# Kernel optimization log

Hardware: AMD Instinct MI355X
Metric: run time of the kernel (lower is better)

Reference implementation:

```python
import jax, jax.numpy as jnp
import numpy as np
from jax import lax

B, T, SDIM, ADIM, HDIM, NH, NBLK, MAXT = 4, 512, 64, 32, 512, 8, 6, 4096
DFF = 4 * HDIM
S = 3 * T  # (num_state_tokens + 1) * context_len
DH = HDIM // NH


def _layernorm(x, g, b, eps=1e-5):
    m = jnp.mean(x, axis=-1, keepdims=True)
    v = jnp.mean((x - m) ** 2, axis=-1, keepdims=True)
    return (x - m) * lax.rsqrt(v + eps) * g + b


def setup_inputs() -> dict:
    key = jax.random.key(0)
    ks = iter(jax.random.split(key, 40))

    def nrm(shape, scale=0.02):
        return jax.random.normal(next(ks), shape, jnp.float32) * scale

    inp = {
        "timesteps": jax.random.randint(next(ks), (B, T), 0, MAXT),
        "state_0": jax.random.normal(next(ks), (B, T, SDIM), jnp.float32),
        "state_1": jax.random.normal(next(ks), (B, T, SDIM), jnp.float32),
        "actions": jax.random.normal(next(ks), (B, T, ADIM), jnp.float32),
        # embeddings / input projections
        "time_emb": nrm((MAXT, HDIM)),
        "Ws": nrm((SDIM, HDIM)), "bs": jnp.zeros((HDIM,), jnp.float32),
        "Wa": nrm((ADIM, HDIM)), "ba": jnp.zeros((HDIM,), jnp.float32),
        # stacked per-block transformer params (leading axis = n_blocks)
        "Wq": nrm((NBLK, HDIM, HDIM)), "bq": jnp.zeros((NBLK, HDIM), jnp.float32),
        "Wk": nrm((NBLK, HDIM, HDIM)), "bk": jnp.zeros((NBLK, HDIM), jnp.float32),
        "Wv": nrm((NBLK, HDIM, HDIM)), "bv": jnp.zeros((NBLK, HDIM), jnp.float32),
        "Wo": nrm((NBLK, HDIM, HDIM)), "bo": jnp.zeros((NBLK, HDIM), jnp.float32),
        "W1": nrm((NBLK, HDIM, DFF)), "b1": jnp.zeros((NBLK, DFF), jnp.float32),
        "W2": nrm((NBLK, DFF, HDIM)), "b2": jnp.zeros((NBLK, HDIM), jnp.float32),
        "ln1_g": jnp.ones((NBLK, HDIM), jnp.float32), "ln1_b": jnp.zeros((NBLK, HDIM), jnp.float32),
        "ln2_g": jnp.ones((NBLK, HDIM), jnp.float32), "ln2_b": jnp.zeros((NBLK, HDIM), jnp.float32),
        # embed layernorm + action head
        "eln_g": jnp.ones((HDIM,), jnp.float32), "eln_b": jnp.zeros((HDIM,), jnp.float32),
        "Wp": nrm((HDIM, ADIM)), "bp": jnp.zeros((ADIM,), jnp.float32),
    }
    return inp


def reference(timesteps, state_0, state_1, actions, time_emb, Ws, bs, Wa, ba,
              Wq, bq, Wk, bk, Wv, bv, Wo, bo, W1, b1, W2, b2,
              ln1_g, ln1_b, ln2_g, ln2_b, eln_g, eln_b, Wp, bp):
    te = time_emb[timesteps]                       # (B, T, H)
    s0 = state_0 @ Ws + bs + te                    # shared state embedding
    s1 = state_1 @ Ws + bs + te
    ae = actions @ Wa + ba + te
    # interleave: (B, T, 3, H) -> (B, 3T, H), token order [s0, s1, a] per timestep
    h = jnp.stack([s0, s1, ae], axis=2).reshape(B, S, HDIM)
    h = _layernorm(h, eln_g, eln_b)

    causal = jnp.tril(jnp.ones((S, S), dtype=bool))
    scale = 1.0 / float(DH) ** 0.5

    def block(x, p):
        wq, bq_, wk, bk_, wv, bv_, wo, bo_, w1, b1_, w2, b2_, g1, be1, g2, be2 = p
        q = (x @ wq + bq_).reshape(B, S, NH, DH)
        k = (x @ wk + bk_).reshape(B, S, NH, DH)
        v = (x @ wv + bv_).reshape(B, S, NH, DH)
        scores = jnp.einsum('bihd,bjhd->bhij', q, k) * scale
        scores = jnp.where(causal, scores, -jnp.inf)
        attn = jax.nn.softmax(scores, axis=-1)
        ctx = jnp.einsum('bhij,bjhd->bihd', attn, v).reshape(B, S, HDIM)
        x = x + (ctx @ wo + bo_)
        x = _layernorm(x, g1, be1)
        mlp = jax.nn.gelu(x @ w1 + b1_, approximate=False) @ w2 + b2_
        x = _layernorm(x + mlp, g2, be2)
        return x, None

    h, _ = lax.scan(block, h,
                    (Wq, bq, Wk, bk, Wv, bv, Wo, bo, W1, b1, W2, b2,
                     ln1_g, ln1_b, ln2_g, ln2_b))

    h = h.reshape(B, T, 3, HDIM)                   # (B, T, num_tokens, H)
    act_in = h[:, :, 1]                            # token index -2 = last state token
    return act_in @ Wp + bp                        # (B, T, act_dim)
```

## Files before the change

### kernel.cpp

```cpp
#include <hip/hip_runtime.h>
#include <hip/hip_bf16.h>
#include <math.h>

#define BB 4
#define TT 512
#define SDIM 64
#define ADIM 32
#define HDIM 512
#define NH 8
#define NBLK 6
#define DFF 2048
#define SS 1536
#define DH 64
#define MS (BB*SS)

typedef __attribute__((ext_vector_type(8))) __bf16 bf16x8;
typedef __attribute__((ext_vector_type(4))) float f32x4;

__device__ __forceinline__ __bf16 f2b(float x) { return (__bf16)x; }

__device__ __forceinline__ void gll16(const void* g, void* l) {
    __builtin_amdgcn_global_load_lds(
        (const __attribute__((address_space(1))) unsigned int*)g,
        (__attribute__((address_space(3))) unsigned int*)l, 16, 0, 0);
}

__global__ __launch_bounds__(512) void embed_ln_kernel(
    const int* __restrict__ timesteps,
    const float* __restrict__ state0, const float* __restrict__ state1,
    const float* __restrict__ actions, const float* __restrict__ time_emb,
    const float* __restrict__ Ws, const float* __restrict__ bs,
    const float* __restrict__ Wa, const float* __restrict__ ba,
    const float* __restrict__ eg, const float* __restrict__ eb,
    __bf16* __restrict__ h_bf)
{
    __shared__ float xs[8][64];
    __shared__ float acc_s[8][512];
    __shared__ int tss[8];
    int c = blockIdx.x, t = blockIdx.y, b = blockIdx.z;
    int i0 = c * 8;
    int tid = threadIdx.x;
    int K = (t == 2) ? ADIM : SDIM;
    int ksh = (t == 2) ? 5 : 6;
    const float* W    = (t == 2) ? Wa : Ws;
    const float* bias = (t == 2) ? ba : bs;
    const float* src  = (t == 0) ? state0  + ((size_t)(b*TT + i0)) * SDIM
                      : (t == 1) ? state1  + ((size_t)(b*TT + i0)) * SDIM
                                 : actions + ((size_t)(b*TT + i0)) * ADIM;

    if (tid < 8) tss[tid] = timesteps[b*TT + i0 + tid];
    for (int idx = tid; idx < 8 * K; idx += 512) {
        int r = idx >> ksh, kk = idx & (K - 1);
        xs[r][kk] = src[r * K + kk];
    }
    __syncthreads();

    float acc[8];
    #pragma unroll
    for (int r = 0; r < 8; ++r)
        acc[r] = bias[tid] + time_emb[(size_t)tss[r] * HDIM + tid];
    for (int kk = 0; kk < K; ++kk) {
        float w = W[(size_t)kk * HDIM + tid];
        #pragma unroll
        for (int r = 0; r < 8; ++r) acc[r] += xs[r][kk] * w;
    }
    #pragma unroll
    for (int r = 0; r < 8; ++r) acc_s[r][tid] = acc[r];
    __syncthreads();

    int w = tid >> 6, lane = tid & 63;
    float4 p0 = *(const float4*)&acc_s[w][lane * 8];
    float4 p1 = *(const float4*)&acc_s[w][lane * 8 + 4];
    float v[8] = {p0.x, p0.y, p0.z, p0.w, p1.x, p1.y, p1.z, p1.w};
    float s = 0.f, sq = 0.f;
    #pragma unroll
    for (int u = 0; u < 8; ++u) { s += v[u]; sq += v[u] * v[u]; }
    #pragma unroll
    for (int off = 1; off < 64; off <<= 1) { s += __shfl_xor(s, off); sq += __shfl_xor(sq, off); }
    float mean = s * (1.f / HDIM);
    float var  = sq * (1.f / HDIM) - mean * mean;
    float inv  = rsqrtf(var + 1e-5f);
    float4 g0 = *(const float4*)(eg + lane * 8), g1 = *(const float4*)(eg + lane * 8 + 4);
    float4 b0 = *(const float4*)(eb + lane * 8), b1 = *(const float4*)(eb + lane * 8 + 4);
    float gg[8] = {g0.x, g0.y, g0.z, g0.w, g1.x, g1.y, g1.z, g1.w};
    float bbv[8] = {b0.x, b0.y, b0.z, b0.w, b1.x, b1.y, b1.z, b1.w};
    __bf16 o8[8];
    #pragma unroll
    for (int u = 0; u < 8; ++u) o8[u] = f2b((v[u] - mean) * inv * gg[u] + bbv[u]);
    int row = b * SS + (i0 + w) * 3 + t;
    *(uint4*)(h_bf + (size_t)row * HDIM + lane * 8) = *(uint4*)o8;
}

template<bool TWO>
__global__ __launch_bounds__(256) void ln_add_kernel(
    __bf16* __restrict__ h_bf, const __bf16* __restrict__ ya,
    const __bf16* __restrict__ yb,
    const float* __restrict__ g, const float* __restrict__ bvec)
{
    int w = threadIdx.x >> 6, lane = threadIdx.x & 63;
    int row = blockIdx.x * 4 + w;
    size_t base = (size_t)row * HDIM + lane * 8;
    bf16x8 h8 = *(const bf16x8*)(h_bf + base);
    bf16x8 a8 = *(const bf16x8*)(ya + base);
    bf16x8 b8;
    if (TWO) b8 = *(const bf16x8*)(yb + base);
    float v[8], s = 0.f, sq = 0.f;
    #pragma unroll
    for (int u = 0; u < 8; ++u) {
        v[u] = (float)h8[u] + (float)a8[u] + (TWO ? (float)b8[u] : 0.f);
        s += v[u]; sq += v[u] * v[u];
    }
    #pragma unroll
    for (int off = 1; off < 64; off <<= 1) { s += __shfl_xor(s, off); sq += __shfl_xor(sq, off); }
    float mean = s * (1.f / HDIM);
    float var  = sq * (1.f / HDIM) - mean * mean;
    float inv  = rsqrtf(var + 1e-5f);
    float4 g0 = *(const float4*)(g + lane * 8), g1 = *(const float4*)(g + lane * 8 + 4);
    float4 b0 = *(const float4*)(bvec + lane * 8), b1 = *(const float4*)(bvec + lane * 8 + 4);
    float gg[8] = {g0.x, g0.y, g0.z, g0.w, g1.x, g1.y, g1.z, g1.w};
    float bbv[8] = {b0.x, b0.y, b0.z, b0.w, b1.x, b1.y, b1.z, b1.w};
    __bf16 o8[8];
    #pragma unroll
    for (int u = 0; u < 8; ++u) o8[u] = f2b((v[u] - mean) * inv * gg[u] + bbv[u]);
    *(uint4*)(h_bf + base) = *(uint4*)o8;
}

__global__ __launch_bounds__(256) void pack_kernel(
    const float* __restrict__ Wq, const float* __restrict__ Wk,
    const float* __restrict__ Wv, const float* __restrict__ Wo,
    const float* __restrict__ W1, const float* __restrict__ W2,
    const float* __restrict__ bq_, const float* __restrict__ bk_, const float* __restrict__ bv_,
    __bf16* __restrict__ wqkvT, __bf16* __restrict__ woT,
    __bf16* __restrict__ w1T, __bf16* __restrict__ w2T, float* __restrict__ biasq)
{
    int lyr = blockIdx.y;
    const float* wq = Wq + (size_t)lyr * HDIM * HDIM;
    const float* wk = Wk + (size_t)lyr * HDIM * HDIM;
    const float* wv = Wv + (size_t)lyr * HDIM * HDIM;
    const float* wo = Wo + (size_t)lyr * HDIM * HDIM;
    const float* w1 = W1 + (size_t)lyr * HDIM * DFF;
    const float* w2 = W2 + (size_t)lyr * DFF * HDIM;
    const float* bqL = bq_ + (size_t)lyr * HDIM;
    const float* bkL = bk_ + (size_t)lyr * HDIM;
    const float* bvL = bv_ + (size_t)lyr * HDIM;
    wqkvT += (size_t)lyr * 1536 * 512;
    woT   += (size_t)lyr * 512 * 512;
    w1T   += (size_t)lyr * 2048 * 512;
    w2T   += (size_t)lyr * 512 * 2048;
    biasq += (size_t)lyr * 1536;

    int bid = blockIdx.x;
    int tid = threadIdx.x;
    if (bid == 768) {
        for (int i = tid; i < 1536; i += 256)
            biasq[i] = (i < 512) ? bqL[i] : ((i < 1024) ? bkL[i-512] : bvL[i-1024]);
        return;
    }
    __shared__ float Ls[64][65];
    const float* src; __bf16* dst; int K, N, kt, nt;
    if (bid < 192) {
        int sec = bid / 64, t = bid % 64;
        src = (sec == 0) ? wq : (sec == 1) ? wk : wv;
        dst = wqkvT + (size_t)sec * 512 * 512;
        K = 512; N = 512; nt = t >> 3; kt = t & 7;
    } else if (bid < 256) {
        int t = bid - 192; src = wo; dst = woT; K = 512; N = 512; nt = t >> 3; kt = t & 7;
    } else if (bid < 512) {
        int t = bid - 256; src = w1; dst = w1T; K = 512; N = 2048; nt = t >> 3; kt = t & 7;
    } else {
        int t = bid - 512; src = w2; dst = w2T; K = 2048; N = 512; nt = t & 7; kt = t >> 3;
    }
    int k0 = kt * 64, n0 = nt * 64;
    int rr = tid >> 4, cc = (tid & 15) * 4;
    #pragma unroll
    for (int p = 0; p < 4; ++p) {
        float4 v = *(const float4*)(src + (size_t)(k0 + rr + p*16) * N + n0 + cc);
        Ls[rr + p*16][cc] = v.x; Ls[rr + p*16][cc+1] = v.y;
        Ls[rr + p*16][cc+2] = v.z; Ls[rr + p*16][cc+3] = v.w;
    }
    __syncthreads();
    int nn = tid >> 3, kc = (tid & 7) * 8;
    #pragma unroll
    for (int p = 0; p < 2; ++p) {
        __bf16 t8[8];
        #pragma unroll
        for (int t2 = 0; t2 < 8; ++t2) t8[t2] = f2b(Ls[kc + t2][nn + p*32]);
        *(uint4*)(dst + (size_t)(n0 + nn + p*32) * K + k0 + kc) = *(uint4*)t8;
    }
}

template<int MT, bool VTMODE>
__global__ __launch_bounds__(256) void gemm_mfma(
    const __bf16* __restrict__ A, const __bf16* __restrict__ Bt,
    const float* __restrict__ bias, __bf16* __restrict__ C,
    __bf16* __restrict__ VTout,
    int N, int Ksub, int lda, int ldb, int ldc, int gelu, size_t cSplitStride)
{
    constexpr int MI = MT / 32;
    constexpr int SMB = 2*MT*64 + 2*128*64;
    __shared__ __align__(16) char sm[SMB];
    __bf16* As = (__bf16*)sm;
    __bf16* Bs = (__bf16*)(sm + 2*MT*64);
    int tid = threadIdx.x;
    int wave = tid >> 6, lane = tid & 63;
    int l15 = lane & 15, quad = lane >> 4;
    int wy = wave >> 1, wx = wave & 1;
    int m0 = blockIdx.y * MT, n0 = blockIdx.x * 128;
    int zs = blockIdx.z;
    int kbase = zs * Ksub;
    C += (size_t)zs * cSplitStride;

    int srow = lane >> 2;
    int clog = (lane & 3) ^ ((lane >> 3) & 3);
    int pchunk = (quad ^ ((l15 >> 1) & 3)) * 8;

    f32x4 acc[MI][4];
    #pragma unroll
    for (int i = 0; i < MI; ++i)
        #pragma unroll
        for (int j = 0; j < 4; ++j) acc[i][j] = (f32x4){0.f,0.f,0.f,0.f};

    const __bf16* Abase = A  + (size_t)m0 * lda + kbase + clog * 8;
    const __bf16* Bbase = Bt + (size_t)n0 * ldb + kbase + clog * 8;
    int NK = Ksub >> 5;

    #pragma unroll
    for (int q = 0; q < MT/64; ++q) {
        int r0 = (wave * (MT/64) + q) * 16;
        gll16(Abase + (size_t)(r0 + srow) * lda, As + r0*32);
    }
    #pragma unroll
    for (int q = 0; q < 2; ++q) {
        int r0 = (wave * 2 + q) * 16;
        gll16(Bbase + (size_t)(r0 + srow) * ldb, Bs + r0*32);
    }

    for (int kt = 0; kt < NK; ++kt) {
        int buf = kt & 1;
        __syncthreads();
        if (kt + 1 < NK) {
            int k0 = (kt + 1) << 5;
            #pragma unroll
            for (int q = 0; q < MT/64; ++q) {
                int r0 = (wave * (MT/64) + q) * 16;
                gll16(Abase + (size_t)(r0 + srow) * lda + k0, As + ((buf^1)*MT + r0)*32);
            }
            #pragma unroll
            for (int q = 0; q < 2; ++q) {
                int r0 = (wave * 2 + q) * 16;
                gll16(Bbase + (size_t)(r0 + srow) * ldb + k0, Bs + ((buf^1)*128 + r0)*32);
            }
        }
        bf16x8 af[MI], bf[4];
        #pragma unroll
        for (int i = 0; i < MI; ++i)
            af[i] = *(const bf16x8*)&As[(buf*MT + wy*(MT/2) + i*16 + l15)*32 + pchunk];
        #pragma unroll
        for (int j = 0; j < 4; ++j)
            bf[j] = *(const bf16x8*)&Bs[(buf*128 + wx*64 + j*16 + l15)*32 + pchunk];
        #pragma unroll
        for (int i = 0; i < MI; ++i)
            #pragma unroll
            for (int j = 0; j < 4; ++j)
                acc[i][j] = __builtin_amdgcn_mfma_f32_16x16x32_bf16(af[i], bf[j], acc[i][j], 0, 0, 0);
    }

    if (VTMODE && n0 >= 1024) {
        __syncthreads();
        __bf16* T = (__bf16*)sm;
        #pragma unroll
        for (int j = 0; j < 4; ++j) {
            int dl = wx*64 + j*16 + l15;
            float bv = bias[n0 + dl];
            int x31 = dl & 31;
            #pragma unroll
            for (int i = 0; i < MI; ++i) {
                int sc = wy*16 + i*4 + quad;
                int phys = sc ^ x31;
                __bf16 v4[4];
                #pragma unroll
                for (int r = 0; r < 4; ++r) v4[r] = f2b(acc[i][j][r] + bv);
                *(uint2*)(T + dl*128 + phys*4) = *(uint2*)v4;
            }
        }
        __syncthreads();
        int dl = tid >> 1, sh = (tid & 1) * 64;
        int dglob = n0 - 1024 + dl;
        int bb = m0 / SS, srel = m0 - bb*SS;
        __bf16* vb = VTout + ((size_t)(bb*NH + (dglob >> 6)) * 64 + (dglob & 63)) * SS + srel + sh;
        int x31 = dl & 31;
        #pragma unroll
        for (int u = 0; u < 8; ++u) {
            int c0 = (sh >> 2) + u*2;
            uint2 lo = *(const uint2*)(T + dl*128 + ((c0    ) ^ x31)*4);
            uint2 hi = *(const uint2*)(T + dl*128 + ((c0 + 1) ^ x31)*4);
            uint4 o; o.x = lo.x; o.y = lo.y; o.z = hi.x; o.w = hi.y;
            *(uint4*)(vb + u*8) = o;
        }
        return;
    }

    #pragma unroll
    for (int j = 0; j < 4; ++j) {
        int cc = n0 + wx*64 + j*16 + l15;
        float bv = (zs == 0) ? bias[cc] : 0.f;
        #pragma unroll
        for (int i = 0; i < MI; ++i) {
            #pragma unroll
            for (int r = 0; r < 4; ++r) {
                int rr = m0 + wy*(MT/2) + i*16 + quad*4 + r;
                float v = acc[i][j][r] + bv;
                if (gelu) {
                    float u2 = v * (0.7978845608f + 0.0356774081f * v * v);
                    float e  = __builtin_amdgcn_exp2f(u2 * 2.885390082f);
                    v = v * (1.f - __builtin_amdgcn_rcpf(e + 1.f));
                }
                C[(size_t)rr * ldc + cc] = f2b(v);
            }
        }
    }
}

#define SM_C 0.18033688011112042f

__device__ __forceinline__ unsigned pack2bf(float a, float b)
{
    union { __bf16 h[2]; unsigned u; } t;
    t.h[0] = (__bf16)a; t.h[1] = (__bf16)b;
    return t.u;
}

__device__ __forceinline__ bf16x8 ptrans(const float* p0, const float* p1, int lane)
{
    int l15 = lane & 15, quad = lane >> 4;
    unsigned pk0a = pack2bf(p0[0], p0[1]), pk0b = pack2bf(p0[2], p0[3]);
    unsigned pk1a = pack2bf(p1[0], p1[1]), pk1b = pack2bf(p1[2], p1[3]);
    int sA = l15 + (quad & 1) * 32;
    int sB = sA + 16;
    int hi = quad >> 1;
    unsigned a0A = (unsigned)__shfl((int)pk0a, sA);
    unsigned a1A = (unsigned)__shfl((int)pk1a, sA);
    unsigned b0A = (unsigned)__shfl((int)pk0b, sA);
    unsigned b1A = (unsigned)__shfl((int)pk1b, sA);
    unsigned a0B = (unsigned)__shfl((int)pk0a, sB);
    unsigned a1B = (unsigned)__shfl((int)pk1a, sB);
    unsigned b0B = (unsigned)__shfl((int)pk0b, sB);
    unsigned b1B = (unsigned)__shfl((int)pk1b, sB);
    union { unsigned u[4]; bf16x8 v; } pb;
    pb.u[0] = hi ? a1A : a0A;
    pb.u[1] = hi ? b1A : b0A;
    pb.u[2] = hi ? a1B : a0B;
    pb.u[3] = hi ? b1B : b0B;
    return pb.v;
}

__global__ __launch_bounds__(256, 3) void attn_kernel(
    __bf16* qkc, const __bf16* __restrict__ VT)
{
    __shared__ __align__(16) char smem[32768];

    int x = blockIdx.x;
    int region = x >> 8;
    int j = x & 255;
    int i = j >> 5;
    int hb = j & 31;
    int qt = (region == 0) ? (23 - i) : (region == 1) ? (8 + i) : i;
    int h = hb >> 2, b = hb & 3;

    int tid = threadIdx.x;
    int w = tid >> 6, lane = tid & 63;
    int l15 = lane & 15, quad = lane >> 4;
    int qrow0 = qt * 64 + w * 16;

    const __bf16* qp = qkc + (size_t)(b*SS + qrow0 + l15) * 1024 + h*64 + quad*8;
    bf16x8 qf0 = *(const bf16x8*)qp;
    bf16x8 qf1 = *(const bf16x8*)(qp + 32);

    const __bf16* kgbase = qkc + (size_t)(b*SS) * 1024 + 512 + h*64;
    const __bf16* vgbase = VT + (size_t)(b*NH + h) * 64 * SS;
    int srow8 = lane >> 3;
    int clog  = (lane & 7) ^ ((lane >> 3) & 7);
    int sw0 = ((0*4 + quad) ^ (l15 & 7)) * 8;
    int sw1 = ((1*4 + quad) ^ (l15 & 7)) * 8;

    f32x4 o0 = {0.f,0.f,0.f,0.f}, o1 = o0, o2 = o0, o3 = o0;
    float sm_m = -1e30f, sm_l = 0.f;

    int nkt = qt + 1;

    #pragma unroll
    for (int q = 0; q < 2; ++q) {
        int r0 = (w*2 + q) * 8;
        gll16(kgbase + (size_t)(r0 + srow8) * 1024 + clog*8, (__bf16*)smem + r0*64);
        gll16(vgbase + (size_t)(r0 + srow8) * SS   + clog*8, (__bf16*)(smem + 16384) + r0*64);
    }
    __syncthreads();

    for (int jt = 0; jt < nkt; ++jt) {
        int buf = jt & 1;
        const __bf16* Kb = (const __bf16*)(smem + buf * 8192);
        const __bf16* Vb = (const __bf16*)(smem + 16384 + buf * 8192);
        if (jt + 1 < nkt) {
            int kb2 = (jt + 1) * 64;
            __bf16* Kn = (__bf16*)(smem + (buf ^ 1) * 8192);
            __bf16* Vn = (__bf16*)(smem + 16384 + (buf ^ 1) * 8192);
            #pragma unroll
            for (int q = 0; q < 2; ++q) {
                int r0 = (w*2 + q) * 8;
                gll16(kgbase + (size_t)(kb2 + r0 + srow8) * 1024 + clog*8, Kn + r0*64);
                gll16(vgbase + (size_t)(r0 + srow8) * SS + kb2 + clog*8,   Vn + r0*64);
            }
        }
        int kb = jt * 64;

        f32x4 s[4];
        #pragma unroll
        for (int f = 0; f < 4; ++f) {
            bf16x8 k0 = *(const bf16x8*)(Kb + (16*f + l15)*64 + sw0);
            bf16x8 k1 = *(const bf16x8*)(Kb + (16*f + l15)*64 + sw1);
            f32x4 sf = {0.f,0.f,0.f,0.f};
            sf = __builtin_amdgcn_mfma_f32_16x16x32_bf16(k0, qf0, sf, 0, 0, 0);
            sf = __builtin_amdgcn_mfma_f32_16x16x32_bf16(k1, qf1, sf, 0, 0, 0);
            s[f] = sf;
        }

        if (kb + 63 > qrow0) {
            int qrow = qrow0 + l15;
            #pragma unroll
            for (int f = 0; f < 4; ++f)
                #pragma unroll
                for (int r = 0; r < 4; ++r)
                    if (kb + 16*f + quad*4 + r > qrow) s[f][r] = -1e30f;
        }

        float tf[4];
        #pragma unroll
        for (int f = 0; f < 4; ++f)
            tf[f] = fmaxf(fmaxf(s[f][0], s[f][1]), fmaxf(s[f][2], s[f][3]));
        float tm = fmaxf(fmaxf(tf[0], tf[1]), fmaxf(tf[2], tf[3]));
        tm = fmaxf(tm, __shfl_xor(tm, 16));
        tm = fmaxf(tm, __shfl_xor(tm, 32));

        if (!__all(tm <= sm_m + 64.f)) {
            float mnew = fmaxf(sm_m, tm);
            float alpha = __builtin_amdgcn_exp2f((sm_m - mnew) * SM_C);
            sm_l *= alpha;
            o0 *= alpha; o1 *= alpha; o2 *= alpha; o3 *= alpha;
            sm_m = mnew;
        }

        float negmC = -sm_m * SM_C;
        float pp[4][4];
        float rf[4];
        #pragma unroll
        for (int f = 0; f < 4; ++f) {
            #pragma unroll
            for (int r = 0; r < 4; ++r)
                pp[f][r] = __builtin_amdgcn_exp2f(fmaf(s[f][r], SM_C, negmC));
            rf[f] = (pp[f][0] + pp[f][1]) + (pp[f][2] + pp[f][3]);
        }
        float rs = (rf[0] + rf[1]) + (rf[2] + rf[3]);
        rs += __shfl_xor(rs, 16);
        rs += __shfl_xor(rs, 32);
        sm_l += rs;

        bf16x8 pb01 = ptrans(pp[0], pp[1], lane);
        bf16x8 pb23 = ptrans(pp[2], pp[3], lane);

        #pragma unroll
        for (int ii = 0; ii < 4; ++ii) {
            bf16x8 va = *(const bf16x8*)(Vb + (16*ii + l15)*64 + sw0);
            bf16x8 vb = *(const bf16x8*)(Vb + (16*ii + l15)*64 + sw1);
            f32x4* op = (ii == 0) ? &o0 : (ii == 1) ? &o1 : (ii == 2) ? &o2 : &o3;
            *op = __builtin_amdgcn_mfma_f32_16x16x32_bf16(va, pb01, *op, 0, 0, 0);
            *op = __builtin_amdgcn_mfma_f32_16x16x32_bf16(vb, pb23, *op, 0, 0, 0);
        }
        __syncthreads();
    }

    float* otw = (float*)smem + w * 16 * 68;
    float inv = 1.f / sm_l;
    #pragma unroll
    for (int r = 0; r < 4; ++r) {
        otw[l15*68 +  0 + quad*4 + r] = o0[r] * inv;
        otw[l15*68 + 16 + quad*4 + r] = o1[r] * inv;
        otw[l15*68 + 32 + quad*4 + r] = o2[r] * inv;
        otw[l15*68 + 48 + quad*4 + r] = o3[r] * inv;
    }
    asm volatile("s_waitcnt lgkmcnt(0)" ::: "memory");
    int row = lane >> 2, ch = (lane & 3) * 16;
    union { __bf16 hh[16]; uint4 q4[2]; } ob;
    #pragma unroll
    for (int t2 = 0; t2 < 16; ++t2) ob.hh[t2] = f2b(otw[row*68 + ch + t2]);
    __bf16* cp = qkc + (size_t)(b*SS + qrow0 + row) * 1024 + h*64 + ch;
    *(uint4*)cp = ob.q4[0];
    *(uint4*)(cp + 8) = ob.q4[1];
}

__global__ __launch_bounds__(256) void proj_kernel(
    const __bf16* __restrict__ h_bf, const float* __restrict__ Wp,
    const float* __restrict__ bp, float* __restrict__ out)
{
    int rid = blockIdx.x * 8 + (threadIdx.x >> 5);
    int col = threadIdx.x & 31;
    int b = rid / TT, i = rid - b * TT;
    const __bf16* x = h_bf + ((size_t)(b*SS) + 3*i + 1) * HDIM;
    float acc = bp[col];
    for (int k8 = 0; k8 < HDIM/8; ++k8) {
        bf16x8 x8 = *(const bf16x8*)(x + k8*8);
        #pragma unroll
        for (int u = 0; u < 8; ++u)
            acc += (float)x8[u] * Wp[(k8*8 + u) * ADIM + col];
    }
    out[(size_t)rid * ADIM + col] = acc;
}

extern "C" void kernel_launch(void* const* d_in, const int* in_sizes, int n_in,
                              void* d_out, int out_size, void* d_ws, size_t ws_size,
                              hipStream_t stream)
{
    (void)in_sizes; (void)n_in; (void)out_size; (void)ws_size;
    const int*   timesteps = (const int*)  d_in[0];
    const float* state0    = (const float*)d_in[1];
    const float* state1    = (const float*)d_in[2];
    const float* actions   = (const float*)d_in[3];
    const float* time_emb  = (const float*)d_in[4];
    const float* Ws  = (const float*)d_in[5];
    const float* bs  = (const float*)d_in[6];
    const float* Wa  = (const float*)d_in[7];
    const float* ba  = (const float*)d_in[8];
    const float* Wq  = (const float*)d_in[9];
    const float* bq  = (const float*)d_in[10];
    const float* Wk  = (const float*)d_in[11];
    const float* bk  = (const float*)d_in[12];
    const float* Wv  = (const float*)d_in[13];
    const float* bv  = (const float*)d_in[14];
    const float* Wo  = (const float*)d_in[15];
    const float* bo  = (const float*)d_in[16];
    const float* W1  = (const float*)d_in[17];
    const float* b1  = (const float*)d_in[18];
    const float* W2  = (const float*)d_in[19];
    const float* b2  = (const float*)d_in[20];
    const float* ln1g = (const float*)d_in[21];
    const float* ln1b = (const float*)d_in[22];
    const float* ln2g = (const float*)d_in[23];
    const float* ln2b = (const float*)d_in[24];
    const float* elng = (const float*)d_in[25];
    const float* elnb = (const float*)d_in[26];
    const float* Wp   = (const float*)d_in[27];
    const float* bp   = (const float*)d_in[28];
    float* out = (float*)d_out;

    const size_t SZ = (size_t)MS * HDIM;
    char* p = (char*)d_ws;
    __bf16* h_bf = (__bf16*)p;           p += SZ * 2;
    __bf16* qk   = (__bf16*)p;           p += (size_t)MS * 1024 * 2;
    __bf16* VT   = (__bf16*)p;           p += SZ * 2;
                      p += SZ * 2;
    __bf16* tmpA = (__bf16*)p;           p += SZ * 2;
    __bf16* tmpB = (__bf16*)p;           p += SZ * 2;
    __bf16* wqkvT = (__bf16*)p;          p += (size_t)NBLK * 1536 * 512 * 2;
    __bf16* woT   = (__bf16*)p;          p += (size_t)NBLK * 512 * 512 * 2;
    __bf16* w1T   = (__bf16*)p;          p += (size_t)NBLK * 2048 * 512 * 2;
    __bf16* w2T   = (__bf16*)p;          p += (size_t)NBLK * 512 * 2048 * 2;
    float*  biasq = (float*)p;           p += (size_t)NBLK * 1536 * 4;
    __bf16* hid   = qk;

    embed_ln_kernel<<<dim3(TT/8, 3, BB), 512, 0, stream>>>(timesteps, state0, state1, actions,
                                                           time_emb, Ws, bs, Wa, ba, elng, elnb, h_bf);

    pack_kernel<<<dim3(769, NBLK), 256, 0, stream>>>(Wq, Wk, Wv, Wo, W1, W2, bq, bk, bv,
                                                     wqkvT, woT, w1T, w2T, biasq);

    dim3 gQKV(1536/128, MS/128, 1);
    dim3 gO  (512/128,  MS/64, 2);
    dim3 gF1 (2048/128, MS/128, 1);

    for (int lyr = 0; lyr < NBLK; ++lyr) {
        const __bf16* wqkvT_l = wqkvT + (size_t)lyr * 1536 * 512;
        const __bf16* woT_l   = woT   + (size_t)lyr * 512 * 512;
        const __bf16* w1T_l   = w1T   + (size_t)lyr * 2048 * 512;
        const __bf16* w2T_l   = w2T   + (size_t)lyr * 512 * 2048;
        const float*  biasq_l = biasq + (size_t)lyr * 1536;

        gemm_mfma<128, true><<<gQKV, 256, 0, stream>>>(h_bf, wqkvT_l, biasq_l, qk, VT,
                                                       1536, 512, 512, 512, 1024, 0, 0);
        attn_kernel<<<dim3(768), 256, 0, stream>>>(qk, VT);
        gemm_mfma<64, false><<<gO, 256, 0, stream>>>(qk, woT_l, bo + lyr*HDIM, tmpA, nullptr,
                                                     512, 256, 1024, 512, 512, 0, SZ);
        ln_add_kernel<true><<<MS/4, 256, 0, stream>>>(h_bf, tmpA, tmpB,
                                                      ln1g + lyr*HDIM, ln1b + lyr*HDIM);
        gemm_mfma<128, false><<<gF1, 256, 0, stream>>>(h_bf, w1T_l, b1 + lyr*DFF, hid, nullptr,
                                                       2048, 512, 512, 512, 2048, 1, 0);
        gemm_mfma<64, false><<<gO, 256, 0, stream>>>(hid, w2T_l, b2 + lyr*HDIM, tmpA, nullptr,
                                                     512, 1024, 2048, 2048, 512, 0, SZ);
        ln_add_kernel<true><<<MS/4, 256, 0, stream>>>(h_bf, tmpA, tmpB,
                                                      ln2g + lyr*HDIM, ln2b + lyr*HDIM);
    }

    proj_kernel<<<(BB*TT)/8, 256, 0, stream>>>(h_bf, Wp, bp, out);
}
```

Measured before the change: 944.6 us.

## Use 4-way split-K with 128-row tiles for W2 GEMM and defer softmax row-sum reduction

```diff
diff --git a/kernel.cpp b/kernel.cpp
--- a/kernel.cpp
+++ b/kernel.cpp
@@ -13,6 +13,7 @@
 #define SS 1536
 #define DH 64
 #define MS (BB*SS)
+#define SZE ((size_t)MS * HDIM)
 
 typedef __attribute__((ext_vector_type(8))) __bf16 bf16x8;
 typedef __attribute__((ext_vector_type(4))) float f32x4;
@@ -91,24 +92,26 @@
     *(uint4*)(h_bf + (size_t)row * HDIM + lane * 8) = *(uint4*)o8;
 }
 
-template<bool TWO>
+template<int NP>
 __global__ __launch_bounds__(256) void ln_add_kernel(
-    __bf16* __restrict__ h_bf, const __bf16* __restrict__ ya,
-    const __bf16* __restrict__ yb,
+    __bf16* __restrict__ h_bf, const __bf16* __restrict__ parts,
     const float* __restrict__ g, const float* __restrict__ bvec)
 {
     int w = threadIdx.x >> 6, lane = threadIdx.x & 63;
     int row = blockIdx.x * 4 + w;
     size_t base = (size_t)row * HDIM + lane * 8;
     bf16x8 h8 = *(const bf16x8*)(h_bf + base);
-    bf16x8 a8 = *(const bf16x8*)(ya + base);
-    bf16x8 b8;
-    if (TWO) b8 = *(const bf16x8*)(yb + base);
+    bf16x8 p8[NP];
+    #pragma unroll
+    for (int p = 0; p < NP; ++p) p8[p] = *(const bf16x8*)(parts + p * SZE + base);
     float v[8], s = 0.f, sq = 0.f;
     #pragma unroll
     for (int u = 0; u < 8; ++u) {
-        v[u] = (float)h8[u] + (float)a8[u] + (TWO ? (float)b8[u] : 0.f);
-        s += v[u]; sq += v[u] * v[u];
+        float acc = (float)h8[u];
+        #pragma unroll
+        for (int p = 0; p < NP; ++p) acc += (float)p8[p][u];
+        v[u] = acc;
+        s += acc; sq += acc * acc;
     }
     #pragma unroll
     for (int off = 1; off < 64; off <<= 1) { s += __shfl_xor(s, off); sq += __shfl_xor(sq, off); }
@@ -437,11 +440,12 @@
         #pragma unroll
         for (int f = 0; f < 4; ++f)
             tf[f] = fmaxf(fmaxf(s[f][0], s[f][1]), fmaxf(s[f][2], s[f][3]));
-        float tm = fmaxf(fmaxf(tf[0], tf[1]), fmaxf(tf[2], tf[3]));
-        tm = fmaxf(tm, __shfl_xor(tm, 16));
-        tm = fmaxf(tm, __shfl_xor(tm, 32));
-
-        if (!__all(tm <= sm_m + 64.f)) {
+        float tm_lane = fmaxf(fmaxf(tf[0], tf[1]), fmaxf(tf[2], tf[3]));
+
+        if (!__all(tm_lane <= sm_m + 64.f)) {
+            float tm = tm_lane;
+            tm = fmaxf(tm, __shfl_xor(tm, 16));
+            tm = fmaxf(tm, __shfl_xor(tm, 32));
             float mnew = fmaxf(sm_m, tm);
             float alpha = __builtin_amdgcn_exp2f((sm_m - mnew) * SM_C);
             sm_l *= alpha;
@@ -459,10 +463,7 @@
                 pp[f][r] = __builtin_amdgcn_exp2f(fmaf(s[f][r], SM_C, negmC));
             rf[f] = (pp[f][0] + pp[f][1]) + (pp[f][2] + pp[f][3]);
         }
-        float rs = (rf[0] + rf[1]) + (rf[2] + rf[3]);
-        rs += __shfl_xor(rs, 16);
-        rs += __shfl_xor(rs, 32);
-        sm_l += rs;
+        sm_l += (rf[0] + rf[1]) + (rf[2] + rf[3]);
 
         bf16x8 pb01 = ptrans(pp[0], pp[1], lane);
         bf16x8 pb23 = ptrans(pp[2], pp[3], lane);
@@ -478,6 +479,8 @@
         __syncthreads();
     }
 
+    sm_l += __shfl_xor(sm_l, 16);
+    sm_l += __shfl_xor(sm_l, 32);
     float* otw = (float*)smem + w * 16 * 68;
     float inv = 1.f / sm_l;
     #pragma unroll
@@ -551,14 +554,12 @@
     const float* bp   = (const float*)d_in[28];
     float* out = (float*)d_out;
 
-    const size_t SZ = (size_t)MS * HDIM;
     char* p = (char*)d_ws;
-    __bf16* h_bf = (__bf16*)p;           p += SZ * 2;
+    __bf16* h_bf = (__bf16*)p;           p += SZE * 2;
     __bf16* qk   = (__bf16*)p;           p += (size_t)MS * 1024 * 2;
-    __bf16* VT   = (__bf16*)p;           p += SZ * 2;
-                      p += SZ * 2;
-    __bf16* tmpA = (__bf16*)p;           p += SZ * 2;
-    __bf16* tmpB = (__bf16*)p;           p += SZ * 2;
+    __bf16* VT   = (__bf16*)p;           p += SZE * 2;
+                      p += SZE * 2;
+    __bf16* tmp  = (__bf16*)p;           p += SZE * 2 * 4;
     __bf16* wqkvT = (__bf16*)p;          p += (size_t)NBLK * 1536 * 512 * 2;
     __bf16* woT   = (__bf16*)p;          p += (size_t)NBLK * 512 * 512 * 2;
     __bf16* w1T   = (__bf16*)p;          p += (size_t)NBLK * 2048 * 512 * 2;
@@ -573,7 +574,8 @@
                                                      wqkvT, woT, w1T, w2T, biasq);
 
     dim3 gQKV(1536/128, MS/128, 1);
-    dim3 gO  (512/128,  MS/64, 2);
+    dim3 gWO (512/128,  MS/64, 2);
+    dim3 gW2 (512/128,  MS/128, 4);
     dim3 gF1 (2048/128, MS/128, 1);
 
     for (int lyr = 0; lyr < NBLK; ++lyr) {
@@ -586,16 +588,16 @@
         gemm_mfma<128, true><<<gQKV, 256, 0, stream>>>(h_bf, wqkvT_l, biasq_l, qk, VT,
                                                        1536, 512, 512, 512, 1024, 0, 0);
         attn_kernel<<<dim3(768), 256, 0, stream>>>(qk, VT);
-        gemm_mfma<64, false><<<gO, 256, 0, stream>>>(qk, woT_l, bo + lyr*HDIM, tmpA, nullptr,
-                                                     512, 256, 1024, 512, 512, 0, SZ);
-        ln_add_kernel<true><<<MS/4, 256, 0, stream>>>(h_bf, tmpA, tmpB,
-                                                      ln1g + lyr*HDIM, ln1b + lyr*HDIM);
+        gemm_mfma<64, false><<<gWO, 256, 0, stream>>>(qk, woT_l, bo + lyr*HDIM, tmp, nullptr,
+                                                      512, 256, 1024, 512, 512, 0, SZE);
+        ln_add_kernel<2><<<MS/4, 256, 0, stream>>>(h_bf, tmp,
+                                                   ln1g + lyr*HDIM, ln1b + lyr*HDIM);
         gemm_mfma<128, false><<<gF1, 256, 0, stream>>>(h_bf, w1T_l, b1 + lyr*DFF, hid, nullptr,
                                                        2048, 512, 512, 512, 2048, 1, 0);
-        gemm_mfma<64, false><<<gO, 256, 0, stream>>>(hid, w2T_l, b2 + lyr*HDIM, tmpA, nullptr,
-                                                     512, 1024, 2048, 2048, 512, 0, SZ);
-        ln_add_kernel<true><<<MS/4, 256, 0, stream>>>(h_bf, tmpA, tmpB,
-                                                      ln2g + lyr*HDIM, ln2b + lyr*HDIM);
+        gemm_mfma<128, false><<<gW2, 256, 0, stream>>>(hid, w2T_l, b2 + lyr*HDIM, tmp, nullptr,
+                                                       512, 512, 2048, 2048, 512, 0, SZE);
+        ln_add_kernel<4><<<MS/4, 256, 0, stream>>>(h_bf, tmp,
+                                                   ln2g + lyr*HDIM, ln2b + lyr*HDIM);
     }
 
     proj_kernel<<<(BB*TT)/8, 256, 0, stream>>>(h_bf, Wp, bp, out);
```

Result: no change. 945.9 us (+0.1%).
